# Kernel optimization log

Measured on AMD Instinct MI355X. Metric: run time of the kernel, lower is better.

## Reference

```python
import jax, jax.numpy as jnp
import numpy as np

B, T, D, H = 4, 4096, 2048, 128

def setup_inputs() -> dict:
    key = jax.random.key(0)
    k1, k2, k3, k4 = jax.random.split(key, 4)
    scale = 0.02
    return {
        "x": jax.random.normal(k1, (B, T, D), dtype=jnp.float32),
        "Wq": jax.random.normal(k2, (D, H), dtype=jnp.float32) * scale,
        "Wk": jax.random.normal(k3, (D, H), dtype=jnp.float32) * scale,
        "Wv": jax.random.normal(k4, (D, H), dtype=jnp.float32) * scale,
    }

def reference(x, Wq, Wk, Wv):
    # x: [B,T,D]; projections to [B,T,H]
    q = jnp.einsum('btd,dh->bth', x, Wq)
    k = jnp.einsum('btd,dh->bth', x, Wk)
    v = jnp.einsum('btd,dh->bth', x, Wv)
    scale = 1.0 / jnp.sqrt(jnp.asarray(q.shape[-1], q.dtype))
    scores = jnp.einsum('bth,bsh->bts', q, k) * scale  # [B,T,T]
    t = x.shape[1]
    causal = jnp.tril(jnp.ones((t, t), dtype=bool))
    scores = jnp.where(causal, scores, -jnp.inf)
    weights = jax.nn.softmax(scores, axis=-1)
    # dropout p=0.0 (eval) -> identity
    out = jnp.einsum('bts,bsh->bth', weights, v)
    return out
```

## Files before the change

### kernel.cpp

```cpp
#include <hip/hip_runtime.h>
#include <hip/hip_bf16.h>

#define Bq 4
#define Tq 4096
#define Dq 2048
#define Hq 128
#define Mq (Bq*Tq)
#define CHUNK 16

typedef __attribute__((ext_vector_type(8))) short bf16x8;
typedef __attribute__((ext_vector_type(4))) float f32x4;

static __device__ __forceinline__ short bfbits(float f) {
    union { __hip_bfloat16 h; short s; } u;
    u.h = __float2bfloat16(f);
    return u.s;
}
static __device__ __forceinline__ float bf2f(short s) {
    union { unsigned u; float f; } v;
    v.u = ((unsigned)(unsigned short)s) << 16;
    return v.f;
}
#define WAIT_LDS() __builtin_amdgcn_s_waitcnt(0xC07F)

__global__ __launch_bounds__(256, 1) void wt_kernel(
    const float* __restrict__ Wqp,
    const float* __restrict__ Wkp,
    const float* __restrict__ Wvp,
    short* __restrict__ wTg)
{
    __shared__ short trsp[128][136];
    const int kc = blockIdx.x;
    const int w  = blockIdx.y;
    const float* __restrict__ W = (w == 0) ? Wqp : (w == 1) ? Wkp : Wvp;
    const float scale = (w == 0) ? 0.08838834764831843f : 1.0f;
    const int t = threadIdx.x;

    #pragma unroll
    for (int i = 0; i < 16; i++) {
        int idx = t + i * 256;
        int r = idx >> 5, c4 = idx & 31;
        float4 f = *(const float4*)&W[(size_t)(kc * 128 + r) * Hq + c4 * 4];
        trsp[c4 * 4 + 0][r] = bfbits(f.x * scale);
        trsp[c4 * 4 + 1][r] = bfbits(f.y * scale);
        trsp[c4 * 4 + 2][r] = bfbits(f.z * scale);
        trsp[c4 * 4 + 3][r] = bfbits(f.w * scale);
    }
    __syncthreads();
    #pragma unroll
    for (int i = 0; i < 8; i++) {
        int idx = t + i * 256;
        int h = idx >> 4, c8 = idx & 15;
        *(bf16x8*)&wTg[((size_t)w * 128 + h) * Dq + kc * 128 + c8 * 8] =
            *(bf16x8*)&trsp[h][c8 * 8];
    }
}

__global__ __launch_bounds__(256, 2) void qkv_fused_kernel(
    const float* __restrict__ x,
    const short* __restrict__ wTg,
    short* __restrict__ qg,
    short* __restrict__ kg,
    short* __restrict__ vTt)
{
    __shared__ short smem[32 * 72 + 384 * 72];
    short (*xs)[72]  = (short(*)[72])smem;
    short (*wts)[72] = (short(*)[72])(smem + 32 * 72);

    const int m0 = blockIdx.x * 32;

    const int t    = threadIdx.x;
    const int lane = t & 63;
    const int qw   = t >> 6;
    const int l15  = lane & 15;
    const int quad = lane >> 4;

    f32x4 o[2][6];
    #pragma unroll
    for (int mf = 0; mf < 2; mf++)
        #pragma unroll
        for (int j = 0; j < 6; j++) o[mf][j] = (f32x4){0.f, 0.f, 0.f, 0.f};

    const int xr = t >> 3, xc = (t & 7) * 8;

    float4  xreg[2];
    bf16x8  wreg[12];

    {
        const float* src = x + (size_t)(m0 + xr) * Dq + xc;
        xreg[0] = *(const float4*)(src + 0);
        xreg[1] = *(const float4*)(src + 4);
        #pragma unroll
        for (int i = 0; i < 12; i++) {
            int idx = t + i * 256;
            wreg[i] = *(const bf16x8*)&wTg[(size_t)(idx >> 3) * Dq + (idx & 7) * 8];
        }
        bf16x8 v0;
        v0[0] = bfbits(xreg[0].x); v0[1] = bfbits(xreg[0].y);
        v0[2] = bfbits(xreg[0].z); v0[3] = bfbits(xreg[0].w);
        v0[4] = bfbits(xreg[1].x); v0[5] = bfbits(xreg[1].y);
        v0[6] = bfbits(xreg[1].z); v0[7] = bfbits(xreg[1].w);
        *(bf16x8*)&xs[xr][xc] = v0;
        #pragma unroll
        for (int i = 0; i < 12; i++) {
            int idx = t + i * 256;
            *(bf16x8*)&wts[idx >> 3][(idx & 7) * 8] = wreg[i];
        }
    }
    __syncthreads();

    for (int k0 = 0; k0 < Dq; k0 += 64) {
        if (k0 + 64 < Dq) {
            const float* src = x + (size_t)(m0 + xr) * Dq + k0 + 64 + xc;
            xreg[0] = *(const float4*)(src + 0);
            xreg[1] = *(const float4*)(src + 4);
            #pragma unroll
            for (int i = 0; i < 12; i++) {
                int idx = t + i * 256;
                wreg[i] = *(const bf16x8*)&wTg[(size_t)(idx >> 3) * Dq + k0 + 64 + (idx & 7) * 8];
            }
        }

        #pragma unroll
        for (int kk = 0; kk < 2; kk++) {
            bf16x8 a[2], b[6];
            #pragma unroll
            for (int mf = 0; mf < 2; mf++)
                a[mf] = *(bf16x8*)&xs[mf * 16 + l15][kk * 32 + quad * 8];
            #pragma unroll
            for (int j = 0; j < 6; j++)
                b[j] = *(bf16x8*)&wts[qw * 96 + j * 16 + l15][kk * 32 + quad * 8];
            #pragma unroll
            for (int mf = 0; mf < 2; mf++)
                #pragma unroll
                for (int j = 0; j < 6; j++)
                    o[mf][j] = __builtin_amdgcn_mfma_f32_16x16x32_bf16(
                        a[mf], b[j], o[mf][j], 0, 0, 0);
        }
        __syncthreads();
        if (k0 + 64 < Dq) {
            bf16x8 v0;
            v0[0] = bfbits(xreg[0].x); v0[1] = bfbits(xreg[0].y);
            v0[2] = bfbits(xreg[0].z); v0[3] = bfbits(xreg[0].w);
            v0[4] = bfbits(xreg[1].x); v0[5] = bfbits(xreg[1].y);
            v0[6] = bfbits(xreg[1].z); v0[7] = bfbits(xreg[1].w);
            *(bf16x8*)&xs[xr][xc] = v0;
            #pragma unroll
            for (int i = 0; i < 12; i++) {
                int idx = t + i * 256;
                *(bf16x8*)&wts[idx >> 3][(idx & 7) * 8] = wreg[i];
            }
            __syncthreads();
        }
    }

    {
        short (*e64)[264] = (short(*)[264])smem;
        #pragma unroll
        for (int mf = 0; mf < 2; mf++)
            #pragma unroll
            for (int j = 0; j < 6; j++) {
                int n0 = qw * 96 + j * 16;
                if (n0 < 256) {
                    #pragma unroll
                    for (int reg = 0; reg < 4; reg++)
                        e64[mf * 16 + quad * 4 + reg][n0 + l15] = bfbits(o[mf][j][reg]);
                }
            }
        __syncthreads();
        #pragma unroll
        for (int i = 0; i < 4; i++) {
            int idx = t + i * 256;
            int r = idx >> 5, u = idx & 31;
            int n = u * 8;
            bf16x8 val = *(bf16x8*)&e64[r][n];
            short* dst = (n < 128) ? &qg[(size_t)(m0 + r) * Hq + n]
                                   : &kg[(size_t)(m0 + r) * Hq + (n - 128)];
            *(bf16x8*)dst = val;
        }
    }
    __syncthreads();
    {
        short (*e128)[40] = (short(*)[40])smem;
        #pragma unroll
        for (int mf = 0; mf < 2; mf++)
            #pragma unroll
            for (int j = 0; j < 6; j++) {
                int n0 = qw * 96 + j * 16;
                if (n0 >= 256) {
                    short4 pk;
                    pk.x = bfbits(o[mf][j][0]); pk.y = bfbits(o[mf][j][1]);
                    pk.z = bfbits(o[mf][j][2]); pk.w = bfbits(o[mf][j][3]);
                    *(short4*)&e128[(n0 - 256) + l15][mf * 16 + quad * 4] = pk;
                }
            }
        __syncthreads();
        const int bb   = m0 / Tq;
        const int jt   = (m0 % Tq) >> 6;
        const int moff = m0 & 63;
        #pragma unroll
        for (int i = 0; i < 2; i++) {
            int idx = t + i * 256;
            int h = idx >> 2, u = idx & 3;
            *(bf16x8*)&vTt[(((size_t)bb * (Tq / 64) + jt) * 128 + h) * 64 + moff + u * 8] =
                *(bf16x8*)&e128[h][u * 8];
        }
    }
}

__global__ __launch_bounds__(256, 3) void attn_part_kernel(
    const short* __restrict__ qg, const short* __restrict__ kg,
    const short* __restrict__ vTt,
    short* __restrict__ Opart,
    float* __restrict__ lv)
{
    __shared__ short ks_s[64][136];
    __shared__ short vt_s[128][72];
    __shared__ short ps_s[64][72];

    const int qt = blockIdx.x;
    const int b  = blockIdx.y;
    const int c  = blockIdx.z;
    const int q0 = qt * 64;

    const int lo = c * CHUNK;
    const int hi = min(qt + 1, lo + CHUNK);
    if (lo >= hi) return;

    const int t    = threadIdx.x;
    const int lane = t & 63;
    const int qw   = t >> 6;
    const int l15  = lane & 15;
    const int quad = lane >> 4;

    bf16x8 qf[4];
    {
        const short* qsrc = qg + (size_t)(b * Tq + q0 + qw * 16 + l15) * Hq + quad * 8;
        #pragma unroll
        for (int kk = 0; kk < 4; kk++)
            qf[kk] = *(const bf16x8*)(qsrc + kk * 32);
    }

    float lsum[4] = {0.f, 0.f, 0.f, 0.f};
    f32x4 o[8];
    #pragma unroll
    for (int nf = 0; nf < 8; nf++) o[nf] = (f32x4){0.f, 0.f, 0.f, 0.f};

    bf16x8 kreg[4], vreg[4];
    {
        const size_t kbase = (size_t)(b * Tq + lo * 64) * Hq;
        const short* vsrc = vTt + (((size_t)b * (Tq / 64) + lo) * 128) * 64;
        #pragma unroll
        for (int i = 0; i < 4; i++) {
            int idx = t + i * 256;
            kreg[i] = *(const bf16x8*)&kg[kbase + (size_t)(idx >> 4) * Hq + (idx & 15) * 8];
            vreg[i] = *(const bf16x8*)&vsrc[idx * 8];
        }
        #pragma unroll
        for (int i = 0; i < 4; i++) {
            int idx = t + i * 256;
            *(bf16x8*)&ks_s[idx >> 4][(idx & 15) * 8] = kreg[i];
            *(bf16x8*)&vt_s[idx >> 3][(idx & 7) * 8]  = vreg[i];
        }
    }
    __syncthreads();

    for (int jt = lo; jt < hi; jt++) {
        if (jt + 1 < hi) {
            const size_t kbase = (size_t)(b * Tq + (jt + 1) * 64) * Hq;
            const short* vsrc = vTt + (((size_t)b * (Tq / 64) + jt + 1) * 128) * 64;
            #pragma unroll
            for (int i = 0; i < 4; i++) {
                int idx = t + i * 256;
                kreg[i] = *(const bf16x8*)&kg[kbase + (size_t)(idx >> 4) * Hq + (idx & 15) * 8];
                vreg[i] = *(const bf16x8*)&vsrc[idx * 8];
            }
        }

        f32x4 sacc[4];
        #pragma unroll
        for (int nf = 0; nf < 4; nf++) sacc[nf] = (f32x4){0.f, 0.f, 0.f, 0.f};
        #pragma unroll
        for (int kk = 0; kk < 4; kk++) {
            bf16x8 bk[4];
            #pragma unroll
            for (int nf = 0; nf < 4; nf++)
                bk[nf] = *(bf16x8*)&ks_s[nf * 16 + l15][kk * 32 + quad * 8];
            #pragma unroll
            for (int nf = 0; nf < 4; nf++)
                sacc[nf] = __builtin_amdgcn_mfma_f32_16x16x32_bf16(qf[kk], bk[nf], sacc[nf], 0, 0, 0);
        }

        const bool diag = (jt == qt);
        #pragma unroll
        for (int reg = 0; reg < 4; reg++) {
            const int rloc = qw * 16 + quad * 4 + reg;
            #pragma unroll
            for (int nf = 0; nf < 4; nf++) {
                float s = sacc[nf][reg];
                if (diag && (nf * 16 + l15 > rloc)) s = -1e30f;
                float p = __expf(s);
                lsum[reg] += p;
                ps_s[rloc][nf * 16 + l15] = bfbits(p);
            }
        }
        WAIT_LDS();

        #pragma unroll
        for (int ks2 = 0; ks2 < 2; ks2++) {
            bf16x8 ap = *(bf16x8*)&ps_s[qw * 16 + l15][ks2 * 32 + quad * 8];
            bf16x8 bv[8];
            #pragma unroll
            for (int nf = 0; nf < 8; nf++)
                bv[nf] = *(bf16x8*)&vt_s[nf * 16 + l15][ks2 * 32 + quad * 8];
            #pragma unroll
            for (int nf = 0; nf < 8; nf++)
                o[nf] = __builtin_amdgcn_mfma_f32_16x16x32_bf16(ap, bv[nf], o[nf], 0, 0, 0);
        }

        __syncthreads();
        if (jt + 1 < hi) {
            #pragma unroll
            for (int i = 0; i < 4; i++) {
                int idx = t + i * 256;
                *(bf16x8*)&ks_s[idx >> 4][(idx & 15) * 8] = kreg[i];
                *(bf16x8*)&vt_s[idx >> 3][(idx & 7) * 8]  = vreg[i];
            }
            __syncthreads();
        }
    }

    #pragma unroll
    for (int reg = 0; reg < 4; reg++) {
        #pragma unroll
        for (int mm = 8; mm >= 1; mm >>= 1)
            lsum[reg] += __shfl_xor(lsum[reg], mm, 16);
    }
    const size_t zoff = (size_t)c * Mq;
    if (l15 == 0) {
        #pragma unroll
        for (int reg = 0; reg < 4; reg++)
            lv[zoff + (size_t)b * Tq + q0 + qw * 16 + quad * 4 + reg] = lsum[reg];
    }

    __syncthreads();
    short (*epi)[136] = (short(*)[136])&ks_s[0][0];
    #pragma unroll
    for (int nf = 0; nf < 8; nf++)
        #pragma unroll
        for (int reg = 0; reg < 4; reg++)
            epi[qw * 16 + quad * 4 + reg][nf * 16 + l15] = bfbits(o[nf][reg]);
    __syncthreads();
    #pragma unroll
    for (int i = 0; i < 4; i++) {
        int idx = t + i * 256;
        int r = idx >> 4, cc = idx & 15;
        *(bf16x8*)&Opart[(zoff + (size_t)b * Tq + q0 + r) * Hq + cc * 8] =
            *(bf16x8*)&epi[r][cc * 8];
    }
}

__global__ __launch_bounds__(256, 4) void merge_kernel(
    const short* __restrict__ Opart, const float* __restrict__ lv,
    float* __restrict__ outg)
{
    const int t   = threadIdx.x;
    const int row = blockIdx.x * 16 + (t >> 4);
    const int cu  = t & 15;

    const int rl  = row & (Tq - 1);
    const int nch = (rl >> 10) + 1;

    float lsum = 0.f;
    float acc[8] = {};
    for (int cc = 0; cc < nch; cc++) {
        lsum += lv[(size_t)cc * Mq + row];
        bf16x8 oc = *(const bf16x8*)&Opart[((size_t)cc * Mq + row) * Hq + cu * 8];
        #pragma unroll
        for (int j = 0; j < 8; j++) acc[j] += bf2f(oc[j]);
    }
    float inv = 1.0f / lsum;

    float4 r0, r1;
    r0.x = acc[0] * inv; r0.y = acc[1] * inv; r0.z = acc[2] * inv; r0.w = acc[3] * inv;
    r1.x = acc[4] * inv; r1.y = acc[5] * inv; r1.z = acc[6] * inv; r1.w = acc[7] * inv;
    float* dst = &outg[(size_t)row * Hq + cu * 8];
    *(float4*)dst       = r0;
    *(float4*)(dst + 4) = r1;
}

extern "C" void kernel_launch(void* const* d_in, const int* in_sizes, int n_in,
                              void* d_out, int out_size, void* d_ws, size_t ws_size,
                              hipStream_t stream) {
    const float* x   = (const float*)d_in[0];
    const float* Wqp = (const float*)d_in[1];
    const float* Wkp = (const float*)d_in[2];
    const float* Wvp = (const float*)d_in[3];
    float* out = (float*)d_out;

    short* qg    = (short*)d_ws;
    short* kg    = qg  + (size_t)Mq * Hq;
    short* vTt   = kg  + (size_t)Mq * Hq;
    short* Opart = vTt + (size_t)Mq * Hq;
    short* wTg   = Opart;
    float* lv    = (float*)(Opart + (size_t)4 * Mq * Hq);

    wt_kernel<<<dim3(16, 3), dim3(256), 0, stream>>>(Wqp, Wkp, Wvp, wTg);
    qkv_fused_kernel<<<dim3(Mq / 32), dim3(256), 0, stream>>>(x, wTg, qg, kg, vTt);
    attn_part_kernel<<<dim3(Tq / 64, Bq, 4), dim3(256), 0, stream>>>(qg, kg, vTt, Opart, lv);
    merge_kernel<<<dim3(Mq / 16), dim3(256), 0, stream>>>(Opart, lv, out);
}
```

Before: 278.7 us.

## Fuse split-K merge into attention via atomic counters and load x directly

Removes the separate merge kernel. Query tiles with a single KV chunk now write normalized fp32 output directly. Multi-chunk tiles use a per-tile atomic counter so the last-finishing chunk block reduces the partials. In the QKV projection, x is loaded straight from global memory into MFMA A-fragments (converted in registers) instead of staging through LDS, and occupancy is raised to 3 blocks. This trades a kernel launch and an extra pass over the partials for atomics, threadfences, and uncoalesced x loads.

```diff
diff --git a/kernel.cpp b/kernel.cpp
--- a/kernel.cpp
+++ b/kernel.cpp
@@ -21,13 +21,20 @@
     v.u = ((unsigned)(unsigned short)s) << 16;
     return v.f;
 }
+static __device__ __forceinline__ bf16x8 cvt8(float4 a, float4 b) {
+    bf16x8 v;
+    v[0] = bfbits(a.x); v[1] = bfbits(a.y); v[2] = bfbits(a.z); v[3] = bfbits(a.w);
+    v[4] = bfbits(b.x); v[5] = bfbits(b.y); v[6] = bfbits(b.z); v[7] = bfbits(b.w);
+    return v;
+}
 #define WAIT_LDS() __builtin_amdgcn_s_waitcnt(0xC07F)
 
 __global__ __launch_bounds__(256, 1) void wt_kernel(
     const float* __restrict__ Wqp,
     const float* __restrict__ Wkp,
     const float* __restrict__ Wvp,
-    short* __restrict__ wTg)
+    short* __restrict__ wTg,
+    int* __restrict__ cnt)
 {
     __shared__ short trsp[128][136];
     const int kc = blockIdx.x;
@@ -35,6 +42,8 @@
     const float* __restrict__ W = (w == 0) ? Wqp : (w == 1) ? Wkp : Wvp;
     const float scale = (w == 0) ? 0.08838834764831843f : 1.0f;
     const int t = threadIdx.x;
+
+    if (kc == 0 && w == 0) cnt[t] = 0;
 
     #pragma unroll
     for (int i = 0; i < 16; i++) {
@@ -56,16 +65,14 @@
     }
 }
 
-__global__ __launch_bounds__(256, 2) void qkv_fused_kernel(
+__global__ __launch_bounds__(256, 3) void qkv_fused_kernel(
     const float* __restrict__ x,
     const short* __restrict__ wTg,
     short* __restrict__ qg,
     short* __restrict__ kg,
     short* __restrict__ vTt)
 {
-    __shared__ short smem[32 * 72 + 384 * 72];
-    short (*xs)[72]  = (short(*)[72])smem;
-    short (*wts)[72] = (short(*)[72])(smem + 32 * 72);
+    __shared__ short wts[384][68];
 
     const int m0 = blockIdx.x * 32;
 
@@ -81,39 +88,21 @@
         #pragma unroll
         for (int j = 0; j < 6; j++) o[mf][j] = (f32x4){0.f, 0.f, 0.f, 0.f};
 
-    const int xr = t >> 3, xc = (t & 7) * 8;
-
-    float4  xreg[2];
-    bf16x8  wreg[12];
-
-    {
-        const float* src = x + (size_t)(m0 + xr) * Dq + xc;
-        xreg[0] = *(const float4*)(src + 0);
-        xreg[1] = *(const float4*)(src + 4);
-        #pragma unroll
-        for (int i = 0; i < 12; i++) {
-            int idx = t + i * 256;
-            wreg[i] = *(const bf16x8*)&wTg[(size_t)(idx >> 3) * Dq + (idx & 7) * 8];
-        }
-        bf16x8 v0;
-        v0[0] = bfbits(xreg[0].x); v0[1] = bfbits(xreg[0].y);
-        v0[2] = bfbits(xreg[0].z); v0[3] = bfbits(xreg[0].w);
-        v0[4] = bfbits(xreg[1].x); v0[5] = bfbits(xreg[1].y);
-        v0[6] = bfbits(xreg[1].z); v0[7] = bfbits(xreg[1].w);
-        *(bf16x8*)&xs[xr][xc] = v0;
-        #pragma unroll
-        for (int i = 0; i < 12; i++) {
-            int idx = t + i * 256;
-            *(bf16x8*)&wts[idx >> 3][(idx & 7) * 8] = wreg[i];
-        }
+    bf16x8 wreg[12];
+    #pragma unroll
+    for (int i = 0; i < 12; i++) {
+        int idx = t + i * 256;
+        wreg[i] = *(const bf16x8*)&wTg[(size_t)(idx >> 3) * Dq + (idx & 7) * 8];
+    }
+    #pragma unroll
+    for (int i = 0; i < 12; i++) {
+        int idx = t + i * 256;
+        *(bf16x8*)&wts[idx >> 3][(idx & 7) * 8] = wreg[i];
     }
     __syncthreads();
 
     for (int k0 = 0; k0 < Dq; k0 += 64) {
         if (k0 + 64 < Dq) {
-            const float* src = x + (size_t)(m0 + xr) * Dq + k0 + 64 + xc;
-            xreg[0] = *(const float4*)(src + 0);
-            xreg[1] = *(const float4*)(src + 4);
             #pragma unroll
             for (int i = 0; i < 12; i++) {
                 int idx = t + i * 256;
@@ -121,30 +110,34 @@
             }
         }
 
+        bf16x8 af[2][2];
+        #pragma unroll
+        for (int mf = 0; mf < 2; mf++)
+            #pragma unroll
+            for (int kk = 0; kk < 2; kk++) {
+                const float* p = x + (size_t)(m0 + mf * 16 + l15) * Dq
+                               + k0 + kk * 32 + quad * 8;
+                float4 a = *(const float4*)(p);
+                float4 b = *(const float4*)(p + 4);
+                af[mf][kk] = cvt8(a, b);
+            }
+
         #pragma unroll
         for (int kk = 0; kk < 2; kk++) {
-            bf16x8 a[2], b[6];
-            #pragma unroll
-            for (int mf = 0; mf < 2; mf++)
-                a[mf] = *(bf16x8*)&xs[mf * 16 + l15][kk * 32 + quad * 8];
+            bf16x8 bfr[6];
             #pragma unroll
             for (int j = 0; j < 6; j++)
-                b[j] = *(bf16x8*)&wts[qw * 96 + j * 16 + l15][kk * 32 + quad * 8];
+                bfr[j] = *(bf16x8*)&wts[qw * 96 + j * 16 + l15][kk * 32 + quad * 8];
             #pragma unroll
             for (int mf = 0; mf < 2; mf++)
                 #pragma unroll
                 for (int j = 0; j < 6; j++)
                     o[mf][j] = __builtin_amdgcn_mfma_f32_16x16x32_bf16(
-                        a[mf], b[j], o[mf][j], 0, 0, 0);
-        }
+                        af[mf][kk], bfr[j], o[mf][j], 0, 0, 0);
+        }
+
         __syncthreads();
         if (k0 + 64 < Dq) {
-            bf16x8 v0;
-            v0[0] = bfbits(xreg[0].x); v0[1] = bfbits(xreg[0].y);
-            v0[2] = bfbits(xreg[0].z); v0[3] = bfbits(xreg[0].w);
-            v0[4] = bfbits(xreg[1].x); v0[5] = bfbits(xreg[1].y);
-            v0[6] = bfbits(xreg[1].z); v0[7] = bfbits(xreg[1].w);
-            *(bf16x8*)&xs[xr][xc] = v0;
             #pragma unroll
             for (int i = 0; i < 12; i++) {
                 int idx = t + i * 256;
@@ -155,7 +148,7 @@
     }
 
     {
-        short (*e64)[264] = (short(*)[264])smem;
+        short (*e64)[264] = (short(*)[264])&wts[0][0];
         #pragma unroll
         for (int mf = 0; mf < 2; mf++)
             #pragma unroll
@@ -181,7 +174,7 @@
     }
     __syncthreads();
     {
-        short (*e128)[40] = (short(*)[40])smem;
+        short (*e128)[40] = (short(*)[40])&wts[0][0];
         #pragma unroll
         for (int mf = 0; mf < 2; mf++)
             #pragma unroll
@@ -212,11 +205,14 @@
     const short* __restrict__ qg, const short* __restrict__ kg,
     const short* __restrict__ vTt,
     short* __restrict__ Opart,
-    float* __restrict__ lv)
+    float* __restrict__ lv,
+    int* __restrict__ cnt,
+    float* __restrict__ outg)
 {
     __shared__ short ks_s[64][136];
     __shared__ short vt_s[128][72];
     __shared__ short ps_s[64][72];
+    __shared__ int sold;
 
     const int qt = blockIdx.x;
     const int b  = blockIdx.y;
@@ -336,6 +332,21 @@
         for (int mm = 8; mm >= 1; mm >>= 1)
             lsum[reg] += __shfl_xor(lsum[reg], mm, 16);
     }
+
+    const int nch = (qt >> 4) + 1;
+
+    if (nch == 1) {
+        #pragma unroll
+        for (int reg = 0; reg < 4; reg++) {
+            float inv = 1.0f / lsum[reg];
+            size_t row = (size_t)b * Tq + q0 + qw * 16 + quad * 4 + reg;
+            #pragma unroll
+            for (int nf = 0; nf < 8; nf++)
+                outg[row * Hq + nf * 16 + l15] = o[nf][reg] * inv;
+        }
+        return;
+    }
+
     const size_t zoff = (size_t)c * Mq;
     if (l15 == 0) {
         #pragma unroll
@@ -358,35 +369,34 @@
         *(bf16x8*)&Opart[(zoff + (size_t)b * Tq + q0 + r) * Hq + cc * 8] =
             *(bf16x8*)&epi[r][cc * 8];
     }
-}
-
-__global__ __launch_bounds__(256, 4) void merge_kernel(
-    const short* __restrict__ Opart, const float* __restrict__ lv,
-    float* __restrict__ outg)
-{
-    const int t   = threadIdx.x;
-    const int row = blockIdx.x * 16 + (t >> 4);
-    const int cu  = t & 15;
-
-    const int rl  = row & (Tq - 1);
-    const int nch = (rl >> 10) + 1;
-
-    float lsum = 0.f;
-    float acc[8] = {};
-    for (int cc = 0; cc < nch; cc++) {
-        lsum += lv[(size_t)cc * Mq + row];
-        bf16x8 oc = *(const bf16x8*)&Opart[((size_t)cc * Mq + row) * Hq + cu * 8];
-        #pragma unroll
-        for (int j = 0; j < 8; j++) acc[j] += bf2f(oc[j]);
-    }
-    float inv = 1.0f / lsum;
-
-    float4 r0, r1;
-    r0.x = acc[0] * inv; r0.y = acc[1] * inv; r0.z = acc[2] * inv; r0.w = acc[3] * inv;
-    r1.x = acc[4] * inv; r1.y = acc[5] * inv; r1.z = acc[6] * inv; r1.w = acc[7] * inv;
-    float* dst = &outg[(size_t)row * Hq + cu * 8];
-    *(float4*)dst       = r0;
-    *(float4*)(dst + 4) = r1;
+
+    __threadfence();
+    if (t == 0) sold = atomicAdd(&cnt[b * 64 + qt], 1);
+    __syncthreads();
+    if (sold != nch - 1) return;
+    __threadfence();
+
+    #pragma unroll
+    for (int i = 0; i < 4; i++) {
+        int r  = (t >> 4) + i * 16;
+        int cu = t & 15;
+        size_t row = (size_t)b * Tq + q0 + r;
+        float acc[8] = {};
+        float ls = 0.f;
+        for (int cc = 0; cc < nch; cc++) {
+            ls += lv[(size_t)cc * Mq + row];
+            bf16x8 oc = *(const bf16x8*)&Opart[((size_t)cc * Mq + row) * Hq + cu * 8];
+            #pragma unroll
+            for (int j = 0; j < 8; j++) acc[j] += bf2f(oc[j]);
+        }
+        float inv = 1.0f / ls;
+        float4 r0, r1;
+        r0.x = acc[0] * inv; r0.y = acc[1] * inv; r0.z = acc[2] * inv; r0.w = acc[3] * inv;
+        r1.x = acc[4] * inv; r1.y = acc[5] * inv; r1.z = acc[6] * inv; r1.w = acc[7] * inv;
+        float* dst = &outg[row * Hq + cu * 8];
+        *(float4*)dst       = r0;
+        *(float4*)(dst + 4) = r1;
+    }
 }
 
 extern "C" void kernel_launch(void* const* d_in, const int* in_sizes, int n_in,
@@ -404,9 +414,10 @@
     short* Opart = vTt + (size_t)Mq * Hq;
     short* wTg   = Opart;
     float* lv    = (float*)(Opart + (size_t)4 * Mq * Hq);
-
-    wt_kernel<<<dim3(16, 3), dim3(256), 0, stream>>>(Wqp, Wkp, Wvp, wTg);
+    int*   cnt   = (int*)(lv + (size_t)4 * Mq);
+
+    wt_kernel<<<dim3(16, 3), dim3(256), 0, stream>>>(Wqp, Wkp, Wvp, wTg, cnt);
     qkv_fused_kernel<<<dim3(Mq / 32), dim3(256), 0, stream>>>(x, wTg, qg, kg, vTt);
-    attn_part_kernel<<<dim3(Tq / 64, Bq, 4), dim3(256), 0, stream>>>(qg, kg, vTt, Opart, lv);
-    merge_kernel<<<dim3(Mq / 16), dim3(256), 0, stream>>>(Opart, lv, out);
-}
+    attn_part_kernel<<<dim3(Tq / 64, Bq, 4), dim3(256), 0, stream>>>(
+        qg, kg, vTt, Opart, lv, cnt, out);
+}
```

Result: slower. 505.8 us (+81.5%).
